# Optimization experiments

Measured on AMD Instinct MI355X. Metric: run time of the kernel, lower is better.

The kernel has to match this reference:

```python
import jax, jax.numpy as jnp
import numpy as np

B, L, T, H, NL, DFF, DIN = 4096, 64, 256, 8, 4, 1024, 6
HD = T // H
EPS = 1e-9


def setup_inputs() -> dict:
    key = jax.random.key(0)
    ks = jax.random.split(key, 12)
    s = 0.02
    inp = {
        "link_states": jax.random.uniform(ks[0], (B, L, DIN), jnp.float32) * 10.0,
        "link_W1": jax.random.normal(ks[1], (L, DIN, T), jnp.float32) * s,
        "link_b1": jnp.zeros((L, T), jnp.float32),
        "link_W2": jax.random.normal(ks[2], (L, T, T), jnp.float32) * s,
        "link_b2": jnp.zeros((L, T), jnp.float32),
        "Wqkv": jax.random.normal(ks[3], (NL, 3 * T, T), jnp.float32) * s,
        "bqkv": jnp.zeros((NL, 3 * T), jnp.float32),
        "Wo": jax.random.normal(ks[4], (NL, T, T), jnp.float32) * s,
        "bo": jnp.zeros((NL, T), jnp.float32),
        "ln1_g": jnp.ones((NL, T), jnp.float32),
        "ln1_b": jnp.zeros((NL, T), jnp.float32),
        "Wff1": jax.random.normal(ks[5], (NL, DFF, T), jnp.float32) * s,
        "bff1": jnp.zeros((NL, DFF), jnp.float32),
        "Wff2": jax.random.normal(ks[6], (NL, T, DFF), jnp.float32) * s,
        "bff2": jnp.zeros((NL, T), jnp.float32),
        "ln2_g": jnp.ones((NL, T), jnp.float32),
        "ln2_b": jnp.zeros((NL, T), jnp.float32),
        "head_W1": jax.random.normal(ks[7], (T, T), jnp.float32) * s,
        "head_b1": jnp.zeros((T,), jnp.float32),
        "head_W2": jax.random.normal(ks[8], (T, 1), jnp.float32) * s,
        "head_b2": jnp.zeros((1,), jnp.float32),
    }
    return inp


def _layernorm(x, g, b):
    m = x.mean(-1, keepdims=True)
    v = ((x - m) ** 2).mean(-1, keepdims=True)
    return (x - m) * jax.lax.rsqrt(v + 1e-5) * g + b


def _normalize_inputs(x):
    # x: [B, L, 6]
    prop = jnp.clip(x[:, :, 0], 0.0)
    tx = jnp.clip(x[:, :, 1], 0.0)
    sum_pt = prop + tx
    # torch.median returns lower-middle element for even L
    t_ref = jnp.sort(sum_pt, axis=1)[:, (L - 1) // 2][:, None]
    t_ref = jnp.clip(t_ref, 1e-6)
    f0 = prop / t_ref
    f1 = tx / t_ref
    f2 = x[:, :, 2]
    f3 = jnp.log1p(jnp.clip(x[:, :, 3], 0.0))
    f4 = jnp.log1p(jnp.clip(x[:, :, 4], 0.0) / t_ref)
    f5 = jnp.log1p(jnp.clip(x[:, :, 5], 0.0))
    head5 = jnp.stack([f0, f1, f2, f3, f4], axis=-1)  # [B,L,5]
    mean_a = head5.mean(axis=1, keepdims=True)
    std_a = head5.std(axis=1, keepdims=True) + EPS
    head5 = jnp.clip(head5, mean_a - 3.0 * std_a, mean_a + 3.0 * std_a)
    mean = head5.mean(axis=1, keepdims=True)
    std = head5.std(axis=1, keepdims=True) + EPS
    head5 = (head5 - mean) / std
    return jnp.concatenate([head5, f5[:, :, None]], axis=-1)


def _posenc():
    pos = jnp.arange(L, dtype=jnp.float32)[:, None]
    div = jnp.exp(-jnp.log(10000.0) * jnp.arange(0, T, 2, dtype=jnp.float32) / T)
    pe = jnp.zeros((L, T), jnp.float32)
    pe = pe.at[:, 0::2].set(jnp.sin(pos * div))
    pe = pe.at[:, 1::2].set(jnp.cos(pos * div))
    return pe


def _forward(link_states, link_W1, link_b1, link_W2, link_b2, Wqkv, bqkv, Wo, bo,
             ln1_g, ln1_b, Wff1, bff1, Wff2, bff2, ln2_g, ln2_b,
             head_W1, head_b1, head_W2, head_b2):
    x = _normalize_inputs(link_states)  # [B,L,6]
    # per-link (unshared) MLP encoders, batched as grouped matmuls
    h = jax.nn.relu(jnp.einsum('bld,ldt->blt', x, link_W1) + link_b1)
    tok = jnp.einsum('blt,lts->bls', h, link_W2) + link_b2  # [B,L,T]
    y = tok + _posenc()
    scale = 1.0 / np.sqrt(HD)
    for l in range(NL):
        qkv = y @ Wqkv[l].T + bqkv[l]  # [B,L,3T]
        q, k, v = jnp.split(qkv, 3, axis=-1)
        q = q.reshape(B, L, H, HD).transpose(0, 2, 1, 3)
        k = k.reshape(B, L, H, HD).transpose(0, 2, 1, 3)
        v = v.reshape(B, L, H, HD).transpose(0, 2, 1, 3)
        attn = jax.nn.softmax(jnp.einsum('bhqd,bhkd->bhqk', q, k) * scale, axis=-1)
        o = jnp.einsum('bhqk,bhkd->bhqd', attn, v).transpose(0, 2, 1, 3).reshape(B, L, T)
        o = o @ Wo[l].T + bo[l]
        y = _layernorm(y + o, ln1_g[l], ln1_b[l])
        ff = jax.nn.relu(y @ Wff1[l].T + bff1[l]) @ Wff2[l].T + bff2[l]
        y = _layernorm(y + ff, ln2_g[l], ln2_b[l])
    pooled = y.mean(axis=1)  # [B,T]
    hh = jax.nn.relu(pooled @ head_W1 + head_b1)
    values = (hh @ head_W2 + head_b2)[:, 0]  # [B]
    return values


def reference(link_states, link_W1, link_b1, link_W2, link_b2, Wqkv, bqkv, Wo, bo,
              ln1_g, ln1_b, Wff1, bff1, Wff2, bff2, ln2_g, ln2_b,
              head_W1, head_b1, head_W2, head_b2):
    return _forward(link_states, link_W1, link_b1, link_W2, link_b2, Wqkv, bqkv, Wo, bo,
                    ln1_g, ln1_b, Wff1, bff1, Wff2, bff2, ln2_g, ln2_b,
                    head_W1, head_b1, head_W2, head_b2)
```

## Files before the change

### kernel.cpp

```cpp
#include <hip/hip_runtime.h>
#include <cstddef>

#define B_   4096
#define L_   64
#define T_   256
#define H_   8
#define HD_  32
#define NL_  4
#define DFF_ 1024
#define DIN_ 6

typedef unsigned short ushort_t;
typedef __attribute__((ext_vector_type(8))) short bf16x8;
typedef __attribute__((ext_vector_type(4))) float f32x4;

__device__ __forceinline__ float wred_sum(float v) {
#pragma unroll
  for (int off = 32; off >= 1; off >>= 1) v += __shfl_xor(v, off, 64);
  return v;
}
__device__ __forceinline__ ushort_t f2bf(float f) {
  unsigned u = __builtin_bit_cast(unsigned, f);
  u += 0x7fffu + ((u >> 16) & 1u);
  return (ushort_t)(u >> 16);
}
__device__ __forceinline__ float bf2f(ushort_t h) {
  unsigned u = ((unsigned)h) << 16;
  return __builtin_bit_cast(float, u);
}
__device__ __forceinline__ unsigned pk2bf(float a, float b) {
  unsigned r;
  asm volatile("v_cvt_pk_bf16_f32 %0, %1, %2" : "=v"(r) : "v"(a), "v"(b));
  return r;
}
__device__ __forceinline__ void gl16(const ushort_t* g, const ushort_t* l) {
  __builtin_amdgcn_global_load_lds(
      (const __attribute__((address_space(1))) unsigned int*)g,
      (__attribute__((address_space(3))) unsigned int*)l, 16, 0, 0);
}

__global__ __launch_bounds__(256) void normalize_k(const float* __restrict__ xs,
                                                   float* __restrict__ xn) {
  const int w = threadIdx.x >> 6;
  const int b = blockIdx.x * 4 + w;
  const int l = threadIdx.x & 63;
  const float* x = xs + ((size_t)b * L_ + l) * DIN_;
  const float x0 = x[0], x1 = x[1], x2 = x[2], x3 = x[3], x4 = x[4], x5 = x[5];
  const float prop = fmaxf(x0, 0.f), tx = fmaxf(x1, 0.f);
  const float sp = prop + tx;

  __shared__ float sh[4][64];
  __shared__ float med_sh[4];
  sh[w][l] = sp;
  __syncthreads();
  int rk = 0;
#pragma unroll 8
  for (int j = 0; j < 64; ++j) {
    const float vj = sh[w][j];
    rk += (vj < sp) || (vj == sp && j < l);
  }
  if (rk == 31) med_sh[w] = sp;
  __syncthreads();
  const float t_ref = fmaxf(med_sh[w], 1e-6f);

  float f[5];
  f[0] = prop / t_ref;
  f[1] = tx / t_ref;
  f[2] = x2;
  f[3] = log1pf(fmaxf(x3, 0.f));
  f[4] = log1pf(fmaxf(x4, 0.f) / t_ref);
  const float f5 = log1pf(fmaxf(x5, 0.f));

  float* dst = xn + ((size_t)b * L_ + l) * DIN_;
#pragma unroll
  for (int i = 0; i < 5; ++i) {
    float v = f[i];
    float m = wred_sum(v) * (1.f / 64.f);
    float d = v - m;
    float sd = sqrtf(wred_sum(d * d) * (1.f / 64.f)) + 1e-9f;
    const float lo = m - 3.f * sd, hi = m + 3.f * sd;
    const float cv = fminf(fmaxf(v, lo), hi);
    const float m2 = wred_sum(cv) * (1.f / 64.f);
    const float d2 = cv - m2;
    const float sd2 = sqrtf(wred_sum(d2 * d2) * (1.f / 64.f)) + 1e-9f;
    dst[i] = (cv - m2) / sd2;
  }
  dst[5] = f5;
}

__global__ __launch_bounds__(256) void prep_k(
    const float* __restrict__ Wqkv, ushort_t* __restrict__ Wqkv16,
    const float* __restrict__ Wo,   ushort_t* __restrict__ Wo16,
    const float* __restrict__ Wff1, ushort_t* __restrict__ Wff116,
    const float* __restrict__ Wff2, ushort_t* __restrict__ Wff216,
    const float* __restrict__ W2,   ushort_t* __restrict__ W2T16,
    float* __restrict__ pe) {
  long idx = (long)blockIdx.x * 256 + threadIdx.x;
  if (idx < 786432) {
    const int NK = 196608;
    const int z = (int)(idx / NK), r = (int)(idx % NK);
    const int e = r & 7, li = (r >> 3) & 15, t = r >> 7;
    const int ks = t & 31, cb = t >> 5;
    Wqkv16[(size_t)z * NK + r] =
        f2bf(Wqkv[(size_t)z * NK + (size_t)(cb * 16 + li) * 256 + ks * 8 + e]);
    return;
  }
  idx -= 786432;
  if (idx < 262144) {
    const int NK = 65536;
    const int z = (int)(idx / NK), r = (int)(idx % NK);
    const int e = r & 7, li = (r >> 3) & 15, t = r >> 7;
    const int ks = t & 31, cb = t >> 5;
    Wo16[(size_t)z * NK + r] =
        f2bf(Wo[(size_t)z * NK + (size_t)(cb * 16 + li) * 256 + ks * 8 + e]);
    return;
  }
  idx -= 262144;
  if (idx < 1048576) {
    const int NK = 262144;
    const int z = (int)(idx / NK), r = (int)(idx % NK);
    const int e = r & 7, li = (r >> 3) & 15, t = r >> 7;
    const int ks = t & 31, cb = t >> 5;
    Wff116[(size_t)z * NK + r] =
        f2bf(Wff1[(size_t)z * NK + (size_t)(cb * 16 + li) * 256 + ks * 8 + e]);
    return;
  }
  idx -= 1048576;
  if (idx < 1048576) {
    const int NK = 262144;
    const int z = (int)(idx / NK), r = (int)(idx % NK);
    const int e = r & 7, li = (r >> 3) & 15, t = r >> 7;
    const int ks = t & 127, cb = t >> 7;
    Wff216[(size_t)z * NK + r] =
        f2bf(Wff2[(size_t)z * NK + (size_t)(cb * 16 + li) * 1024 + ks * 8 + e]);
    return;
  }
  idx -= 1048576;
  if (idx < 4194304) {
    const int l = (int)(idx >> 16), r = (int)(idx & 65535), s = r >> 8, t = r & 255;
    W2T16[idx] = f2bf(W2[((size_t)l << 16) | (t << 8) | s]);
    return;
  }
  idx -= 4194304;
  if (idx < 8192) {
    const int l = (int)(idx >> 7), i = (int)(idx & 127);
    const float div = expf(-9.210340371976184f * (2.0f * i) / 256.0f);
    const float ang = (float)l * div;
    pe[l * T_ + 2 * i]     = sinf(ang);
    pe[l * T_ + 2 * i + 1] = cosf(ang);
  }
}

__global__ __launch_bounds__(256) void link1_k(const float* __restrict__ xn,
                                               const float* __restrict__ W1,
                                               const float* __restrict__ b1,
                                               ushort_t* __restrict__ h,
                                               int Bc) {
  const size_t r0 = (size_t)blockIdx.x * 16;
  const int col = threadIdx.x;
#pragma unroll
  for (int i = 0; i < 16; ++i) {
    const size_t r = r0 + i;
    const int l = (int)(r & (L_ - 1));
    const size_t bloc = r >> 6;
    const float* x = xn + r * DIN_;
    float a = b1[l * T_ + col];
#pragma unroll
    for (int d = 0; d < DIN_; ++d)
      a = fmaf(x[d], W1[((size_t)l * DIN_ + d) * T_ + col], a);
    h[((size_t)l * Bc + bloc) * T_ + col] = f2bf(fmaxf(a, 0.f));
  }
}

__global__ __launch_bounds__(512) void linkgemm_k(
    const ushort_t* __restrict__ A,
    const ushort_t* __restrict__ W,
    const float* __restrict__ bias,
    const float* __restrict__ pe,
    float* __restrict__ y32, int Bc) {
  __shared__ ushort_t lA[2][4096];
  __shared__ ushort_t lB[2][8192];
  const int tid = threadIdx.x;
  const int lane = tid & 63, w = tid >> 6;
  const int wr = w >> 2, wc = w & 3;
  const size_t b0 = (size_t)blockIdx.x * 128;
  const int l = blockIdx.z;
  const ushort_t* Az = A + ((size_t)l * Bc + b0) * 256;
  const ushort_t* Wz = W + (size_t)l * 65536;

  const int sm = tid >> 6, sks = (tid >> 4) & 3, srr = tid & 15;

  auto stage = [&](int buf, int kt) {
    gl16(Az + (size_t)(16 * sm + srr) * 256 + kt + sks * 8,
         &lA[buf][(tid & ~63) * 8]);
#pragma unroll
    for (int rd = 0; rd < 2; ++rd) {
      const int nb = sm + rd * 8;
      gl16(Wz + (size_t)(nb * 16 + srr) * 256 + kt + sks * 8,
           &lB[buf][rd * 4096 + (tid & ~63) * 8]);
    }
  };

  f32x4 acc[4][4];
#pragma unroll
  for (int mi = 0; mi < 4; ++mi)
#pragma unroll
    for (int ni = 0; ni < 4; ++ni) acc[mi][ni] = (f32x4){0.f, 0.f, 0.f, 0.f};

  stage(0, 0);
  asm volatile("s_waitcnt vmcnt(0)" ::: "memory");
  __syncthreads();
  int cur = 0;
  for (int t = 0; t < 8; ++t) {
    if (t + 1 < 8) stage(cur ^ 1, (t + 1) << 5);
    bf16x8 af[4], bfr[4];
#pragma unroll
    for (int mi = 0; mi < 4; ++mi)
      af[mi] = *(const bf16x8*)&lA[cur][((wr * 4 + mi) * 64 + lane) * 8];
#pragma unroll
    for (int ni = 0; ni < 4; ++ni)
      bfr[ni] = *(const bf16x8*)&lB[cur][((wc * 4 + ni) * 64 + lane) * 8];
#pragma unroll
    for (int mi = 0; mi < 4; ++mi)
#pragma unroll
      for (int ni = 0; ni < 4; ++ni)
        acc[mi][ni] = __builtin_amdgcn_mfma_f32_16x16x32_bf16(
            af[mi], bfr[ni], acc[mi][ni], 0, 0, 0);
    asm volatile("s_waitcnt vmcnt(0)" ::: "memory");
    __syncthreads();
    cur ^= 1;
  }

  const int r_in = (lane >> 4) * 4;
  const int c_in = lane & 15;
#pragma unroll
  for (int ni = 0; ni < 4; ++ni) {
    const int cg = wc * 64 + ni * 16 + c_in;
    const float bs = bias[l * 256 + cg] + pe[l * 256 + cg];
#pragma unroll
    for (int mi = 0; mi < 4; ++mi) {
#pragma unroll
      for (int rg = 0; rg < 4; ++rg) {
        const size_t bg = b0 + wr * 64 + mi * 16 + r_in + rg;
        y32[bg * 16384 + l * 256 + cg] = acc[mi][ni][rg] + bs;
      }
    }
  }
}

template <int LAST>
__global__ __launch_bounds__(256, 2) void layer_k(
    float* __restrict__ y32,
    const ushort_t* __restrict__ Wq, const float* __restrict__ bqkv,
    const ushort_t* __restrict__ Wo, const float* __restrict__ bo,
    const float* __restrict__ ln1g, const float* __restrict__ ln1b,
    const ushort_t* __restrict__ Wf1, const float* __restrict__ bf1,
    const ushort_t* __restrict__ Wf2, const float* __restrict__ bf2,
    const float* __restrict__ ln2g, const float* __restrict__ ln2b,
    float* __restrict__ pool) {
  __shared__ ushort_t yF[16384];
  __shared__ ushort_t sc[18432];
  __shared__ float red[4][2][64];
  const int b = blockIdx.x;
  const int tid = threadIdx.x, lane = tid & 63, w = tid >> 6;
  const int li = lane & 15, g = lane >> 4;
  const size_t row0 = (size_t)b * 64;
  const float scale = 0.17677669529663687f;
  ushort_t* bufw = sc + w * 2304;
  ushort_t* vtw  = sc + 9216 + w * 2304;
  ushort_t* zF   = sc;

#pragma unroll
  for (int j = 0; j < 8; ++j) {
    const int u = j * 256 + tid;
    const int row = u & 63, ks = u >> 6;
    const float* src = y32 + (row0 + row) * 256 + ks * 8;
    const float4 a = *(const float4*)src;
    const float4 c = *(const float4*)(src + 4);
    uint4 v;
    v.x = pk2bf(a.x, a.y);
    v.y = pk2bf(a.z, a.w);
    v.z = pk2bf(c.x, c.y);
    v.w = pk2bf(c.z, c.w);
    *(uint4*)&yF[(((row >> 4) * 32 + ks) * 16 + (row & 15)) * 8] = v;
  }
  __syncthreads();

  f32x4 oa2[2][4][2];
#pragma unroll
  for (int hi = 0; hi < 2; ++hi) {
    const int h = w * 2 + hi, hoff = h * 32;

    f32x4 acc[3][2][4];
#pragma unroll
    for (int m = 0; m < 3; ++m)
#pragma unroll
      for (int n = 0; n < 2; ++n)
#pragma unroll
        for (int mi = 0; mi < 4; ++mi) acc[m][n][mi] = (f32x4){0.f, 0.f, 0.f, 0.f};
    __builtin_amdgcn_s_setprio(1);
#pragma unroll
    for (int kt = 0; kt < 8; ++kt) {
      bf16x8 af[4];
#pragma unroll
      for (int mi = 0; mi < 4; ++mi)
        af[mi] = *(const bf16x8*)&yF[((mi * 32 + kt * 4 + g) * 16 + li) * 8];
      bf16x8 bw[3][2];
#pragma unroll
      for (int m = 0; m < 3; ++m)
#pragma unroll
        for (int n = 0; n < 2; ++n)
          bw[m][n] = *(const bf16x8*)(Wq +
              (size_t)(((m * 16 + 2 * h + n) * 32 + kt * 4 + g) * 16 + li) * 8);
#pragma unroll
      for (int m = 0; m < 3; ++m)
#pragma unroll
        for (int n = 0; n < 2; ++n)
#pragma unroll
          for (int mi = 0; mi < 4; ++mi)
            acc[m][n][mi] = __builtin_amdgcn_mfma_f32_16x16x32_bf16(
                af[mi], bw[m][n], acc[m][n][mi], 0, 0, 0);
    }
    __builtin_amdgcn_s_setprio(0);
    float bs[3][2];
#pragma unroll
    for (int m = 0; m < 3; ++m)
#pragma unroll
      for (int n = 0; n < 2; ++n) bs[m][n] = bqkv[m * 256 + hoff + 16 * n + li];

#pragma unroll
    for (int n = 0; n < 2; ++n)
#pragma unroll
      for (int mi = 0; mi < 4; ++mi) {
        const unsigned p0 = pk2bf(acc[0][n][mi][0] + bs[0][n],
                                  acc[0][n][mi][1] + bs[0][n]);
        const unsigned p1 = pk2bf(acc[0][n][mi][2] + bs[0][n],
                                  acc[0][n][mi][3] + bs[0][n]);
        const int base = (16 * mi + 4 * g) * 36 + 16 * n + li;
        bufw[base]       = (ushort_t)p0;
        bufw[base + 36]  = (ushort_t)(p0 >> 16);
        bufw[base + 72]  = (ushort_t)p1;
        bufw[base + 108] = (ushort_t)(p1 >> 16);
      }
    bf16x8 qb[4];
#pragma unroll
    for (int ni = 0; ni < 4; ++ni)
      qb[ni] = *(const bf16x8*)&bufw[(16 * ni + li) * 36 + g * 8];

#pragma unroll
    for (int n = 0; n < 2; ++n)
#pragma unroll
      for (int mi = 0; mi < 4; ++mi) {
        const unsigned p0 = pk2bf(acc[1][n][mi][0] + bs[1][n],
                                  acc[1][n][mi][1] + bs[1][n]);
        const unsigned p1 = pk2bf(acc[1][n][mi][2] + bs[1][n],
                                  acc[1][n][mi][3] + bs[1][n]);
        const int base = (16 * mi + 4 * g) * 36 + 16 * n + li;
        bufw[base]       = (ushort_t)p0;
        bufw[base + 36]  = (ushort_t)(p0 >> 16);
        bufw[base + 72]  = (ushort_t)p1;
        bufw[base + 108] = (ushort_t)(p1 >> 16);
      }
    bf16x8 ka[4];
#pragma unroll
    for (int mi = 0; mi < 4; ++mi)
      ka[mi] = *(const bf16x8*)&bufw[(16 * mi + li) * 36 + g * 8];

#pragma unroll
    for (int n = 0; n < 2; ++n)
#pragma unroll
      for (int mi = 0; mi < 4; ++mi) {
        const unsigned p0 = pk2bf(acc[2][n][mi][0] + bs[2][n],
                                  acc[2][n][mi][1] + bs[2][n]);
        const unsigned p1 = pk2bf(acc[2][n][mi][2] + bs[2][n],
                                  acc[2][n][mi][3] + bs[2][n]);
        *(uint2*)&vtw[(16 * n + li) * 72 + 16 * mi + 4 * g] = make_uint2(p0, p1);
      }
    bf16x8 vb[2][2];
#pragma unroll
    for (int ks = 0; ks < 2; ++ks)
#pragma unroll
      for (int n2 = 0; n2 < 2; ++n2)
        vb[ks][n2] = *(const bf16x8*)&vtw[(16 * n2 + li) * 72 + ks * 32 + g * 8];

#pragma unroll
    for (int mi = 0; mi < 4; ++mi)
#pragma unroll
      for (int n2 = 0; n2 < 2; ++n2) oa2[hi][mi][n2] = (f32x4){0.f, 0.f, 0.f, 0.f};

#pragma unroll
    for (int half = 0; half < 2; ++half) {
      f32x4 s[4][2];
      __builtin_amdgcn_s_setprio(1);
#pragma unroll
      for (int mi = 0; mi < 4; ++mi)
#pragma unroll
        for (int nn = 0; nn < 2; ++nn)
          s[mi][nn] = __builtin_amdgcn_mfma_f32_16x16x32_bf16(
              ka[mi], qb[2 * half + nn], (f32x4){0.f, 0.f, 0.f, 0.f}, 0, 0, 0);
      __builtin_amdgcn_s_setprio(0);

#pragma unroll
      for (int nn = 0; nn < 2; ++nn) {
        float mx = -3.4e38f;
#pragma unroll
        for (int mi = 0; mi < 4; ++mi)
#pragma unroll
          for (int r = 0; r < 4; ++r) {
            s[mi][nn][r] *= scale;
            mx = fmaxf(mx, s[mi][nn][r]);
          }
        mx = fmaxf(mx, __shfl_xor(mx, 16, 64));
        mx = fmaxf(mx, __shfl_xor(mx, 32, 64));
        float sum = 0.f;
#pragma unroll
        for (int mi = 0; mi < 4; ++mi)
#pragma unroll
          for (int r = 0; r < 4; ++r) {
            const float e = expf(s[mi][nn][r] - mx);
            s[mi][nn][r] = e;
            sum += e;
          }
        sum += __shfl_xor(sum, 16, 64);
        sum += __shfl_xor(sum, 32, 64);
        const float inv = 1.f / sum;
        const int qrow = 16 * nn + li;
#pragma unroll
        for (int mi = 0; mi < 4; ++mi) {
          const unsigned lo = pk2bf(s[mi][nn][0] * inv, s[mi][nn][1] * inv);
          const unsigned hi2 = pk2bf(s[mi][nn][2] * inv, s[mi][nn][3] * inv);
          *(uint2*)&bufw[qrow * 72 + 16 * mi + 4 * g] = make_uint2(lo, hi2);
        }
      }

      __builtin_amdgcn_s_setprio(1);
#pragma unroll
      for (int ks = 0; ks < 2; ++ks) {
        bf16x8 pa[2];
#pragma unroll
        for (int m2 = 0; m2 < 2; ++m2)
          pa[m2] = *(const bf16x8*)&bufw[(16 * m2 + li) * 72 + ks * 32 + g * 8];
#pragma unroll
        for (int m2 = 0; m2 < 2; ++m2)
#pragma unroll
          for (int n2 = 0; n2 < 2; ++n2)
            oa2[hi][2 * half + m2][n2] = __builtin_amdgcn_mfma_f32_16x16x32_bf16(
                pa[m2], vb[ks][n2], oa2[hi][2 * half + m2][n2], 0, 0, 0);
      }
      __builtin_amdgcn_s_setprio(0);
    }
  }

  __syncthreads();
#pragma unroll
  for (int hi = 0; hi < 2; ++hi) {
    const int hoff = (2 * w + hi) * 32;
#pragma unroll
    for (int mi = 0; mi < 4; ++mi)
#pragma unroll
      for (int n2 = 0; n2 < 2; ++n2) {
        const unsigned p0 = pk2bf(oa2[hi][mi][n2][0], oa2[hi][mi][n2][1]);
        const unsigned p1 = pk2bf(oa2[hi][mi][n2][2], oa2[hi][mi][n2][3]);
        const int col = hoff + 16 * n2 + li;
        const int base = ((mi * 32 + (col >> 3)) * 16 + 4 * g) * 8 + (col & 7);
        yF[base]      = (ushort_t)p0;
        yF[base + 8]  = (ushort_t)(p0 >> 16);
        yF[base + 16] = (ushort_t)p1;
        yF[base + 24] = (ushort_t)(p1 >> 16);
      }
  }
  __syncthreads();

  f32x4 acc[4][4];
#pragma unroll
  for (int mi = 0; mi < 4; ++mi)
#pragma unroll
    for (int ni = 0; ni < 4; ++ni) acc[mi][ni] = (f32x4){0.f, 0.f, 0.f, 0.f};
  __builtin_amdgcn_s_setprio(1);
#pragma unroll
  for (int kt = 0; kt < 8; ++kt) {
    bf16x8 af[4], bfr[4];
#pragma unroll
    for (int mi = 0; mi < 4; ++mi)
      af[mi] = *(const bf16x8*)&yF[((mi * 32 + kt * 4 + g) * 16 + li) * 8];
#pragma unroll
    for (int ni = 0; ni < 4; ++ni)
      bfr[ni] = *(const bf16x8*)(Wo +
          (size_t)(((4 * w + ni) * 32 + kt * 4 + g) * 16 + li) * 8);
#pragma unroll
    for (int mi = 0; mi < 4; ++mi)
#pragma unroll
      for (int ni = 0; ni < 4; ++ni)
        acc[mi][ni] = __builtin_amdgcn_mfma_f32_16x16x32_bf16(
            af[mi], bfr[ni], acc[mi][ni], 0, 0, 0);
  }
  __builtin_amdgcn_s_setprio(0);

  const int r_in = (lane >> 4) * 4;
  const int c_in = lane & 15;
  float y1r[4][4][4];
#pragma unroll
  for (int mi = 0; mi < 4; ++mi) {
#pragma unroll
    for (int rg = 0; rg < 4; ++rg) {
      const int row_l = 16 * mi + r_in + rg;
      float s1 = 0.f, s2 = 0.f;
#pragma unroll
      for (int ni = 0; ni < 4; ++ni) {
        const int cg = 64 * w + 16 * ni + c_in;
        const float zv = acc[mi][ni][rg] + bo[cg] + y32[(row0 + row_l) * 256 + cg];
        acc[mi][ni][rg] = zv;
        s1 += zv;
        s2 += zv * zv;
      }
#pragma unroll
      for (int off = 1; off <= 8; off <<= 1) {
        s1 += __shfl_xor(s1, off, 64);
        s2 += __shfl_xor(s2, off, 64);
      }
      if (c_in == 0) {
        red[w][0][row_l] = s1;
        red[w][1][row_l] = s2;
      }
    }
  }
  __syncthreads();
#pragma unroll
  for (int mi = 0; mi < 4; ++mi) {
#pragma unroll
    for (int rg = 0; rg < 4; ++rg) {
      const int row_l = 16 * mi + r_in + rg;
      const float S1 = red[0][0][row_l] + red[1][0][row_l] + red[2][0][row_l] + red[3][0][row_l];
      const float S2 = red[0][1][row_l] + red[1][1][row_l] + red[2][1][row_l] + red[3][1][row_l];
      const float m = S1 * (1.f / 256.f);
      const float var = S2 * (1.f / 256.f) - m * m;
      const float rs = rsqrtf(var + 1e-5f);
      float tv[4];
#pragma unroll
      for (int ni = 0; ni < 4; ++ni) {
        const int cg = 64 * w + 16 * ni + c_in;
        tv[ni] = (acc[mi][ni][rg] - m) * rs * ln1g[cg] + ln1b[cg];
        y1r[mi][ni][rg] = tv[ni];
      }
      const unsigned p0 = pk2bf(tv[0], tv[1]);
      const unsigned p1 = pk2bf(tv[2], tv[3]);
#pragma unroll
      for (int ni = 0; ni < 4; ++ni) {
        const int cg = 64 * w + 16 * ni + c_in;
        const unsigned pk = (ni < 2) ? p0 : p1;
        const ushort_t hv = (ni & 1) ? (ushort_t)(pk >> 16) : (ushort_t)pk;
        yF[((mi * 32 + (cg >> 3)) * 16 + (row_l & 15)) * 8 + (cg & 7)] = hv;
      }
    }
  }
  __syncthreads();

  f32x4 acc2[4][4];
#pragma unroll
  for (int mi = 0; mi < 4; ++mi)
#pragma unroll
    for (int ni = 0; ni < 4; ++ni) acc2[mi][ni] = (f32x4){0.f, 0.f, 0.f, 0.f};

#pragma unroll 1
  for (int q = 0; q < 4; ++q) {
#pragma unroll 1
    for (int p = 0; p < 2; ++p) {
      f32x4 acc1[4][2];
#pragma unroll
      for (int mi = 0; mi < 4; ++mi)
#pragma unroll
        for (int n = 0; n < 2; ++n) acc1[mi][n] = (f32x4){0.f, 0.f, 0.f, 0.f};
      __builtin_amdgcn_s_setprio(1);
#pragma unroll
      for (int kt = 0; kt < 8; ++kt) {
        bf16x8 af[4], bw[2];
#pragma unroll
        for (int mi = 0; mi < 4; ++mi)
          af[mi] = *(const bf16x8*)&yF[((mi * 32 + kt * 4 + g) * 16 + li) * 8];
#pragma unroll
        for (int n = 0; n < 2; ++n)
          bw[n] = *(const bf16x8*)(Wf1 +
              (size_t)(((16 * q + 4 * w + 2 * p + n) * 32 + kt * 4 + g) * 16 + li) * 8);
#pragma unroll
        for (int mi = 0; mi < 4; ++mi)
#pragma unroll
          for (int n = 0; n < 2; ++n)
            acc1[mi][n] = __builtin_amdgcn_mfma_f32_16x16x32_bf16(
                af[mi], bw[n], acc1[mi][n], 0, 0, 0);
      }
      __builtin_amdgcn_s_setprio(0);
      if (q && p == 0) __syncthreads();
#pragma unroll
      for (int n = 0; n < 2; ++n) {
        const int kk = 64 * w + 32 * p + 16 * n + li;
        const float bb = bf1[256 * q + kk];
#pragma unroll
        for (int mi = 0; mi < 4; ++mi) {
          const unsigned p0 = pk2bf(fmaxf(acc1[mi][n][0] + bb, 0.f),
                                    fmaxf(acc1[mi][n][1] + bb, 0.f));
          const unsigned p1 = pk2bf(fmaxf(acc1[mi][n][2] + bb, 0.f),
                                    fmaxf(acc1[mi][n][3] + bb, 0.f));
          const int base = ((mi * 32 + (kk >> 3)) * 16 + 4 * g) * 8 + (kk & 7);
          zF[base]      = (ushort_t)p0;
          zF[base + 8]  = (ushort_t)(p0 >> 16);
          zF[base + 16] = (ushort_t)p1;
          zF[base + 24] = (ushort_t)(p1 >> 16);
        }
      }
    }
    __syncthreads();
    __builtin_amdgcn_s_setprio(1);
#pragma unroll
    for (int kt = 0; kt < 8; ++kt) {
      bf16x8 af2[4], bw2[4];
#pragma unroll
      for (int mi = 0; mi < 4; ++mi)
        af2[mi] = *(const bf16x8*)&zF[((mi * 32 + kt * 4 + g) * 16 + li) * 8];
#pragma unroll
      for (int ni = 0; ni < 4; ++ni)
        bw2[ni] = *(const bf16x8*)(Wf2 +
            (size_t)(((4 * w + ni) * 128 + 32 * q + kt * 4 + g) * 16 + li) * 8);
#pragma unroll
      for (int mi = 0; mi < 4; ++mi)
#pragma unroll
        for (int ni = 0; ni < 4; ++ni)
          acc2[mi][ni] = __builtin_amdgcn_mfma_f32_16x16x32_bf16(
              af2[mi], bw2[ni], acc2[mi][ni], 0, 0, 0);
    }
    __builtin_amdgcn_s_setprio(0);
  }

#pragma unroll
  for (int mi = 0; mi < 4; ++mi) {
#pragma unroll
    for (int rg = 0; rg < 4; ++rg) {
      const int row_l = 16 * mi + r_in + rg;
      float s1 = 0.f, s2 = 0.f;
#pragma unroll
      for (int ni = 0; ni < 4; ++ni) {
        const int cg = 64 * w + 16 * ni + c_in;
        const float zv = acc2[mi][ni][rg] + bf2[cg] + y1r[mi][ni][rg];
        acc2[mi][ni][rg] = zv;
        s1 += zv;
        s2 += zv * zv;
      }
#pragma unroll
      for (int off = 1; off <= 8; off <<= 1) {
        s1 += __shfl_xor(s1, off, 64);
        s2 += __shfl_xor(s2, off, 64);
      }
      if (c_in == 0) {
        red[w][0][row_l] = s1;
        red[w][1][row_l] = s2;
      }
    }
  }
  __syncthreads();
  float colsum[4] = {0.f, 0.f, 0.f, 0.f};
#pragma unroll
  for (int mi = 0; mi < 4; ++mi) {
#pragma unroll
    for (int rg = 0; rg < 4; ++rg) {
      const int row_l = 16 * mi + r_in + rg;
      const float S1 = red[0][0][row_l] + red[1][0][row_l] + red[2][0][row_l] + red[3][0][row_l];
      const float S2 = red[0][1][row_l] + red[1][1][row_l] + red[2][1][row_l] + red[3][1][row_l];
      const float m = S1 * (1.f / 256.f);
      const float var = S2 * (1.f / 256.f) - m * m;
      const float rs = rsqrtf(var + 1e-5f);
#pragma unroll
      for (int ni = 0; ni < 4; ++ni) {
        const int cg = 64 * w + 16 * ni + c_in;
        const float v = (acc2[mi][ni][rg] - m) * rs * ln2g[cg] + ln2b[cg];
        if constexpr (LAST) {
          colsum[ni] += v;
        } else {
          y32[(row0 + row_l) * 256 + cg] = v;
        }
      }
    }
  }
  if constexpr (LAST) {
#pragma unroll
    for (int ni = 0; ni < 4; ++ni) {
      float s = colsum[ni];
      s += __shfl_xor(s, 16, 64);
      s += __shfl_xor(s, 32, 64);
      if (g == 0) pool[(size_t)b * 256 + 64 * w + 16 * ni + c_in] = s * (1.f / 64.f);
    }
  }
}

__global__ __launch_bounds__(256) void headgemm_k(
    const float* __restrict__ A, const float* __restrict__ Wt,
    const float* __restrict__ bias, float* __restrict__ out) {
  const int tid = threadIdx.x;
  const int tx = tid & 63, ty = tid >> 6;
  const int cfull = tx * 4;
  const size_t b0 = (size_t)blockIdx.x * 64;

  __shared__ float At[256][68];

  float4 acc[16];
#pragma unroll
  for (int r = 0; r < 16; ++r) acc[r] = make_float4(0.f, 0.f, 0.f, 0.f);
  const int r0 = ty * 16;

  {
    const int rr = tid >> 6;
    const int k4 = (tid & 63) * 4;
#pragma unroll
    for (int p = 0; p < 16; ++p) {
      const int r = p * 4 + rr;
      const float4 v = *(const float4*)(A + (b0 + r) * 256 + k4);
      At[k4 + 0][r] = v.x;
      At[k4 + 1][r] = v.y;
      At[k4 + 2][r] = v.z;
      At[k4 + 3][r] = v.w;
    }
  }
  __syncthreads();
  const float* wp = Wt + cfull;
#pragma unroll 2
  for (int k = 0; k < 256; ++k) {
    const float4 w = *(const float4*)wp;
    wp += 256;
    const float4* ar = (const float4*)(&At[k][r0]);
    const float4 a0 = ar[0], a1 = ar[1], a2 = ar[2], a3 = ar[3];
    const float av[16] = {a0.x, a0.y, a0.z, a0.w, a1.x, a1.y, a1.z, a1.w,
                          a2.x, a2.y, a2.z, a2.w, a3.x, a3.y, a3.z, a3.w};
#pragma unroll
    for (int r = 0; r < 16; ++r) {
      acc[r].x = fmaf(av[r], w.x, acc[r].x);
      acc[r].y = fmaf(av[r], w.y, acc[r].y);
      acc[r].z = fmaf(av[r], w.z, acc[r].z);
      acc[r].w = fmaf(av[r], w.w, acc[r].w);
    }
  }
  const float4 bb = *(const float4*)(bias + cfull);
#pragma unroll
  for (int r = 0; r < 16; ++r) {
    const size_t row = b0 + r0 + r;
    float4 o;
    o.x = fmaxf(acc[r].x + bb.x, 0.f);
    o.y = fmaxf(acc[r].y + bb.y, 0.f);
    o.z = fmaxf(acc[r].z + bb.z, 0.f);
    o.w = fmaxf(acc[r].w + bb.w, 0.f);
    *(float4*)(out + row * 256 + cfull) = o;
  }
}

__global__ __launch_bounds__(64) void head2_k(const float* __restrict__ hh,
                                              const float* __restrict__ W2,
                                              const float* __restrict__ b2,
                                              float* __restrict__ out) {
  const size_t b = blockIdx.x;
  const int lane = threadIdx.x;
  const float4 hv = *(const float4*)(hh + b * T_ + lane * 4);
  const float4 wv = *(const float4*)(W2 + lane * 4);
  float s = hv.x * wv.x + hv.y * wv.y + hv.z * wv.z + hv.w * wv.w;
  s = wred_sum(s);
  if (lane == 0) out[b] = s + b2[0];
}

extern "C" void kernel_launch(void* const* d_in, const int* in_sizes, int n_in,
                              void* d_out, int out_size, void* d_ws, size_t ws_size,
                              hipStream_t stream) {
  const float* link_states = (const float*)d_in[0];
  const float* link_W1 = (const float*)d_in[1];
  const float* link_b1 = (const float*)d_in[2];
  const float* link_W2 = (const float*)d_in[3];
  const float* link_b2 = (const float*)d_in[4];
  const float* Wqkv = (const float*)d_in[5];
  const float* bqkv = (const float*)d_in[6];
  const float* Wo = (const float*)d_in[7];
  const float* bo = (const float*)d_in[8];
  const float* ln1_g = (const float*)d_in[9];
  const float* ln1_b = (const float*)d_in[10];
  const float* Wff1 = (const float*)d_in[11];
  const float* bff1 = (const float*)d_in[12];
  const float* Wff2 = (const float*)d_in[13];
  const float* bff2 = (const float*)d_in[14];
  const float* ln2_g = (const float*)d_in[15];
  const float* ln2_b = (const float*)d_in[16];
  const float* head_W1 = (const float*)d_in[17];
  const float* head_b1 = (const float*)d_in[18];
  const float* head_W2 = (const float*)d_in[19];
  const float* head_b2 = (const float*)d_in[20];

  char* base = (char*)d_ws;
  size_t off = 0;
  auto alloc = [&](size_t bytes) -> char* {
    char* p = base + off;
    off = (off + bytes + 255) & ~(size_t)255;
    return p;
  };

  ushort_t* Wqkv16 = (ushort_t*)alloc((size_t)NL_ * 768 * 256 * 2);
  ushort_t* Wo16   = (ushort_t*)alloc((size_t)NL_ * 256 * 256 * 2);
  ushort_t* Wff116 = (ushort_t*)alloc((size_t)NL_ * 1024 * 256 * 2);
  ushort_t* Wff216 = (ushort_t*)alloc((size_t)NL_ * 256 * 1024 * 2);
  ushort_t* W2T16  = (ushort_t*)alloc((size_t)L_ * 256 * 256 * 2);
  float* pe     = (float*)alloc((size_t)L_ * T_ * 4);
  float* xn     = (float*)alloc((size_t)B_ * L_ * DIN_ * 4);
  float* pooled = (float*)alloc((size_t)B_ * T_ * 4);
  float* hh     = (float*)alloc((size_t)B_ * T_ * 4);

  const size_t fixed_end = off;
  const size_t availB = (ws_size > fixed_end + 65536) ? (ws_size - fixed_end - 65536) : 0;
  int NC = 1;
  while (NC < 32 && (size_t)(B_ / NC) * 98304ull > availB) NC <<= 1;
  const int Bc = B_ / NC;

  float*    y32  = (float*)alloc((size_t)Bc * L_ * T_ * 4);
  ushort_t* hbuf = (ushort_t*)alloc((size_t)Bc * L_ * T_ * 2);

  prep_k<<<28704, 256, 0, stream>>>(Wqkv, Wqkv16, Wo, Wo16, Wff1, Wff116,
                                    Wff2, Wff216, link_W2, W2T16, pe);
  normalize_k<<<B_ / 4, 256, 0, stream>>>(link_states, xn);

  for (int c = 0; c < NC; ++c) {
    const size_t bs = (size_t)c * Bc;

    link1_k<<<(Bc * L_) / 16, 256, 0, stream>>>(xn + bs * L_ * DIN_, link_W1,
                                                link_b1, hbuf, Bc);
    linkgemm_k<<<dim3(Bc / 128, 1, L_), 512, 0, stream>>>(
        hbuf, W2T16, link_b2, pe, y32, Bc);

    for (int l = 0; l < NL_ - 1; ++l) {
      layer_k<0><<<dim3(Bc, 1, 1), 256, 0, stream>>>(
          y32,
          Wqkv16 + (size_t)l * 768 * 256, bqkv + l * 768,
          Wo16 + (size_t)l * 256 * 256, bo + l * 256,
          ln1_g + l * 256, ln1_b + l * 256,
          Wff116 + (size_t)l * 1024 * 256, bff1 + l * 1024,
          Wff216 + (size_t)l * 256 * 1024, bff2 + l * 256,
          ln2_g + l * 256, ln2_b + l * 256, nullptr);
    }
    {
      const int l = NL_ - 1;
      layer_k<1><<<dim3(Bc, 1, 1), 256, 0, stream>>>(
          y32,
          Wqkv16 + (size_t)l * 768 * 256, bqkv + l * 768,
          Wo16 + (size_t)l * 256 * 256, bo + l * 256,
          ln1_g + l * 256, ln1_b + l * 256,
          Wff116 + (size_t)l * 1024 * 256, bff1 + l * 1024,
          Wff216 + (size_t)l * 256 * 1024, bff2 + l * 256,
          ln2_g + l * 256, ln2_b + l * 256, pooled + bs * T_);
    }
  }

  headgemm_k<<<B_ / 64, 256, 0, stream>>>(pooled, head_W1, head_b1, hh);
  head2_k<<<B_, 64, 0, stream>>>(hh, head_W2, head_b2, (float*)d_out);
}
```

Before: 3.527 ms.

## Fuse pairs of transformer layers into one kernel keeping activations on-chip

Merges two consecutive encoder layers into a single kernel launch. Between the two layers the residual stream stays in registers (yres) and in the bf16 LDS tile, so the fp32 activation round trip through global memory between layers is avoided, and the launch count halves. The cost is higher register pressure from holding the residual in registers across the whole layer, which under the 2-blocks-per-CU launch bound may cause spills.

Measured after the change: 6.624 ms. +87.8%, slower.

```diff
diff --git a/kernel.cpp b/kernel.cpp
--- a/kernel.cpp
+++ b/kernel.cpp
@@ -249,14 +249,14 @@
 }
 
 template <int LAST>
-__global__ __launch_bounds__(256, 2) void layer_k(
+__global__ __launch_bounds__(256, 2) void layers2_k(
     float* __restrict__ y32,
-    const ushort_t* __restrict__ Wq, const float* __restrict__ bqkv,
-    const ushort_t* __restrict__ Wo, const float* __restrict__ bo,
-    const float* __restrict__ ln1g, const float* __restrict__ ln1b,
-    const ushort_t* __restrict__ Wf1, const float* __restrict__ bf1,
-    const ushort_t* __restrict__ Wf2, const float* __restrict__ bf2,
-    const float* __restrict__ ln2g, const float* __restrict__ ln2b,
+    const ushort_t* __restrict__ Wq0, const float* __restrict__ bqkv0,
+    const ushort_t* __restrict__ Wo0, const float* __restrict__ bo0,
+    const float* __restrict__ ln1g0, const float* __restrict__ ln1b0,
+    const ushort_t* __restrict__ Wf10, const float* __restrict__ bf10,
+    const ushort_t* __restrict__ Wf20, const float* __restrict__ bf20,
+    const float* __restrict__ ln2g0, const float* __restrict__ ln2b0,
     float* __restrict__ pool) {
   __shared__ ushort_t yF[16384];
   __shared__ ushort_t sc[18432];
@@ -270,6 +270,9 @@
   ushort_t* vtw  = sc + 9216 + w * 2304;
   ushort_t* zF   = sc;
 
+  const int r_in = (lane >> 4) * 4;
+  const int c_in = lane & 15;
+
 #pragma unroll
   for (int j = 0; j < 8; ++j) {
     const int u = j * 256 + tid;
@@ -284,408 +287,465 @@
     v.w = pk2bf(c.z, c.w);
     *(uint4*)&yF[(((row >> 4) * 32 + ks) * 16 + (row & 15)) * 8] = v;
   }
+  float yres[4][4][4];
+#pragma unroll
+  for (int mi = 0; mi < 4; ++mi)
+#pragma unroll
+    for (int rg = 0; rg < 4; ++rg) {
+      const int row_l = 16 * mi + r_in + rg;
+#pragma unroll
+      for (int ni = 0; ni < 4; ++ni) {
+        const int cg = 64 * w + 16 * ni + c_in;
+        yres[mi][ni][rg] = y32[(row0 + row_l) * 256 + cg];
+      }
+    }
   __syncthreads();
 
-  f32x4 oa2[2][4][2];
-#pragma unroll
-  for (int hi = 0; hi < 2; ++hi) {
-    const int h = w * 2 + hi, hoff = h * 32;
-
-    f32x4 acc[3][2][4];
-#pragma unroll
-    for (int m = 0; m < 3; ++m)
+#pragma unroll 1
+  for (int l2 = 0; l2 < 2; ++l2) {
+    const ushort_t* Wq   = Wq0  + (size_t)l2 * 768 * 256;
+    const float*    bqkv = bqkv0 + l2 * 768;
+    const ushort_t* Wo   = Wo0  + (size_t)l2 * 256 * 256;
+    const float*    bo   = bo0  + l2 * 256;
+    const float*    ln1g = ln1g0 + l2 * 256;
+    const float*    ln1b = ln1b0 + l2 * 256;
+    const ushort_t* Wf1  = Wf10 + (size_t)l2 * 1024 * 256;
+    const float*    bf1  = bf10 + l2 * 1024;
+    const ushort_t* Wf2  = Wf20 + (size_t)l2 * 256 * 1024;
+    const float*    bf2  = bf20 + l2 * 256;
+    const float*    ln2g = ln2g0 + l2 * 256;
+    const float*    ln2b = ln2b0 + l2 * 256;
+
+    f32x4 oa2[2][4][2];
+#pragma unroll
+    for (int hi = 0; hi < 2; ++hi) {
+      const int h = w * 2 + hi, hoff = h * 32;
+
+      f32x4 acc[3][2][4];
+#pragma unroll
+      for (int m = 0; m < 3; ++m)
+#pragma unroll
+        for (int n = 0; n < 2; ++n)
+#pragma unroll
+          for (int mi = 0; mi < 4; ++mi) acc[m][n][mi] = (f32x4){0.f, 0.f, 0.f, 0.f};
+      __builtin_amdgcn_s_setprio(1);
+#pragma unroll
+      for (int kt = 0; kt < 8; ++kt) {
+        bf16x8 af[4];
+#pragma unroll
+        for (int mi = 0; mi < 4; ++mi)
+          af[mi] = *(const bf16x8*)&yF[((mi * 32 + kt * 4 + g) * 16 + li) * 8];
+        bf16x8 bw[3][2];
+#pragma unroll
+        for (int m = 0; m < 3; ++m)
+#pragma unroll
+          for (int n = 0; n < 2; ++n)
+            bw[m][n] = *(const bf16x8*)(Wq +
+                (size_t)(((m * 16 + 2 * h + n) * 32 + kt * 4 + g) * 16 + li) * 8);
+#pragma unroll
+        for (int m = 0; m < 3; ++m)
+#pragma unroll
+          for (int n = 0; n < 2; ++n)
+#pragma unroll
+            for (int mi = 0; mi < 4; ++mi)
+              acc[m][n][mi] = __builtin_amdgcn_mfma_f32_16x16x32_bf16(
+                  af[mi], bw[m][n], acc[m][n][mi], 0, 0, 0);
+      }
+      __builtin_amdgcn_s_setprio(0);
+      float bs[3][2];
+#pragma unroll
+      for (int m = 0; m < 3; ++m)
+#pragma unroll
+        for (int n = 0; n < 2; ++n) bs[m][n] = bqkv[m * 256 + hoff + 16 * n + li];
+
 #pragma unroll
       for (int n = 0; n < 2; ++n)
 #pragma unroll
-        for (int mi = 0; mi < 4; ++mi) acc[m][n][mi] = (f32x4){0.f, 0.f, 0.f, 0.f};
+        for (int mi = 0; mi < 4; ++mi) {
+          const unsigned p0 = pk2bf(acc[0][n][mi][0] + bs[0][n],
+                                    acc[0][n][mi][1] + bs[0][n]);
+          const unsigned p1 = pk2bf(acc[0][n][mi][2] + bs[0][n],
+                                    acc[0][n][mi][3] + bs[0][n]);
+          const int base = (16 * mi + 4 * g) * 36 + 16 * n + li;
+          bufw[base]       = (ushort_t)p0;
+          bufw[base + 36]  = (ushort_t)(p0 >> 16);
+          bufw[base + 72]  = (ushort_t)p1;
+          bufw[base + 108] = (ushort_t)(p1 >> 16);
+        }
+      bf16x8 qb[4];
+#pragma unroll
+      for (int ni = 0; ni < 4; ++ni)
+        qb[ni] = *(const bf16x8*)&bufw[(16 * ni + li) * 36 + g * 8];
+
+#pragma unroll
+      for (int n = 0; n < 2; ++n)
+#pragma unroll
+        for (int mi = 0; mi < 4; ++mi) {
+          const unsigned p0 = pk2bf(acc[1][n][mi][0] + bs[1][n],
+                                    acc[1][n][mi][1] + bs[1][n]);
+          const unsigned p1 = pk2bf(acc[1][n][mi][2] + bs[1][n],
+                                    acc[1][n][mi][3] + bs[1][n]);
+          const int base = (16 * mi + 4 * g) * 36 + 16 * n + li;
+          bufw[base]       = (ushort_t)p0;
+          bufw[base + 36]  = (ushort_t)(p0 >> 16);
+          bufw[base + 72]  = (ushort_t)p1;
+          bufw[base + 108] = (ushort_t)(p1 >> 16);
+        }
+      bf16x8 ka[4];
+#pragma unroll
+      for (int mi = 0; mi < 4; ++mi)
+        ka[mi] = *(const bf16x8*)&bufw[(16 * mi + li) * 36 + g * 8];
+
+#pragma unroll
+      for (int n = 0; n < 2; ++n)
+#pragma unroll
+        for (int mi = 0; mi < 4; ++mi) {
+          const unsigned p0 = pk2bf(acc[2][n][mi][0] + bs[2][n],
+                                    acc[2][n][mi][1] + bs[2][n]);
+          const unsigned p1 = pk2bf(acc[2][n][mi][2] + bs[2][n],
+                                    acc[2][n][mi][3] + bs[2][n]);
+          *(uint2*)&vtw[(16 * n + li) * 72 + 16 * mi + 4 * g] = make_uint2(p0, p1);
+        }
+      bf16x8 vb[2][2];
+#pragma unroll
+      for (int ks = 0; ks < 2; ++ks)
+#pragma unroll
+        for (int n2 = 0; n2 < 2; ++n2)
+          vb[ks][n2] = *(const bf16x8*)&vtw[(16 * n2 + li) * 72 + ks * 32 + g * 8];
+
+#pragma unroll
+      for (int mi = 0; mi < 4; ++mi)
+#pragma unroll
+        for (int n2 = 0; n2 < 2; ++n2) oa2[hi][mi][n2] = (f32x4){0.f, 0.f, 0.f, 0.f};
+
+#pragma unroll
+      for (int half = 0; half < 2; ++half) {
+        f32x4 s[4][2];
+        __builtin_amdgcn_s_setprio(1);
+#pragma unroll
+        for (int mi = 0; mi < 4; ++mi)
+#pragma unroll
+          for (int nn = 0; nn < 2; ++nn)
+            s[mi][nn] = __builtin_amdgcn_mfma_f32_16x16x32_bf16(
+                ka[mi], qb[2 * half + nn], (f32x4){0.f, 0.f, 0.f, 0.f}, 0, 0, 0);
+        __builtin_amdgcn_s_setprio(0);
+
+#pragma unroll
+        for (int nn = 0; nn < 2; ++nn) {
+          float mx = -3.4e38f;
+#pragma unroll
+          for (int mi = 0; mi < 4; ++mi)
+#pragma unroll
+            for (int r = 0; r < 4; ++r) {
+              s[mi][nn][r] *= scale;
+              mx = fmaxf(mx, s[mi][nn][r]);
+            }
+          mx = fmaxf(mx, __shfl_xor(mx, 16, 64));
+          mx = fmaxf(mx, __shfl_xor(mx, 32, 64));
+          float sum = 0.f;
+#pragma unroll
+          for (int mi = 0; mi < 4; ++mi)
+#pragma unroll
+            for (int r = 0; r < 4; ++r) {
+              const float e = expf(s[mi][nn][r] - mx);
+              s[mi][nn][r] = e;
+              sum += e;
+            }
+          sum += __shfl_xor(sum, 16, 64);
+          sum += __shfl_xor(sum, 32, 64);
+          const float inv = 1.f / sum;
+          const int qrow = 16 * nn + li;
+#pragma unroll
+          for (int mi = 0; mi < 4; ++mi) {
+            const unsigned lo = pk2bf(s[mi][nn][0] * inv, s[mi][nn][1] * inv);
+            const unsigned hi2 = pk2bf(s[mi][nn][2] * inv, s[mi][nn][3] * inv);
+            *(uint2*)&bufw[qrow * 72 + 16 * mi + 4 * g] = make_uint2(lo, hi2);
+          }
+        }
+
+        __builtin_amdgcn_s_setprio(1);
+#pragma unroll
+        for (int ks = 0; ks < 2; ++ks) {
+          bf16x8 pa[2];
+#pragma unroll
+          for (int m2 = 0; m2 < 2; ++m2)
+            pa[m2] = *(const bf16x8*)&bufw[(16 * m2 + li) * 72 + ks * 32 + g * 8];
+#pragma unroll
+          for (int m2 = 0; m2 < 2; ++m2)
+#pragma unroll
+            for (int n2 = 0; n2 < 2; ++n2)
+              oa2[hi][2 * half + m2][n2] = __builtin_amdgcn_mfma_f32_16x16x32_bf16(
+                  pa[m2], vb[ks][n2], oa2[hi][2 * half + m2][n2], 0, 0, 0);
+        }
+        __builtin_amdgcn_s_setprio(0);
+      }
+    }
+
+    __syncthreads();
+#pragma unroll
+    for (int hi = 0; hi < 2; ++hi) {
+      const int hoff = (2 * w + hi) * 32;
+#pragma unroll
+      for (int mi = 0; mi < 4; ++mi)
+#pragma unroll
+        for (int n2 = 0; n2 < 2; ++n2) {
+          const unsigned p0 = pk2bf(oa2[hi][mi][n2][0], oa2[hi][mi][n2][1]);
+          const unsigned p1 = pk2bf(oa2[hi][mi][n2][2], oa2[hi][mi][n2][3]);
+          const int col = hoff + 16 * n2 + li;
+          const int base = ((mi * 32 + (col >> 3)) * 16 + 4 * g) * 8 + (col & 7);
+          yF[base]      = (ushort_t)p0;
+          yF[base + 8]  = (ushort_t)(p0 >> 16);
+          yF[base + 16] = (ushort_t)p1;
+          yF[base + 24] = (ushort_t)(p1 >> 16);
+        }
+    }
+    __syncthreads();
+
+    f32x4 acc[4][4];
+#pragma unroll
+    for (int mi = 0; mi < 4; ++mi)
+#pragma unroll
+      for (int ni = 0; ni < 4; ++ni) acc[mi][ni] = (f32x4){0.f, 0.f, 0.f, 0.f};
     __builtin_amdgcn_s_setprio(1);
 #pragma unroll
     for (int kt = 0; kt < 8; ++kt) {
-      bf16x8 af[4];
+      bf16x8 af[4], bfr[4];
 #pragma unroll
       for (int mi = 0; mi < 4; ++mi)
         af[mi] = *(const bf16x8*)&yF[((mi * 32 + kt * 4 + g) * 16 + li) * 8];
-      bf16x8 bw[3][2];
-#pragma unroll
-      for (int m = 0; m < 3; ++m)
-#pragma unroll
-        for (int n = 0; n < 2; ++n)
-          bw[m][n] = *(const bf16x8*)(Wq +
-              (size_t)(((m * 16 + 2 * h + n) * 32 + kt * 4 + g) * 16 + li) * 8);
-#pragma unroll
-      for (int m = 0; m < 3; ++m)
-#pragma unroll
-        for (int n = 0; n < 2; ++n)
+#pragma unroll
+      for (int ni = 0; ni < 4; ++ni)
+        bfr[ni] = *(const bf16x8*)(Wo +
+            (size_t)(((4 * w + ni) * 32 + kt * 4 + g) * 16 + li) * 8);
+#pragma unroll
+      for (int mi = 0; mi < 4; ++mi)
+#pragma unroll
+        for (int ni = 0; ni < 4; ++ni)
+          acc[mi][ni] = __builtin_amdgcn_mfma_f32_16x16x32_bf16(
+              af[mi], bfr[ni], acc[mi][ni], 0, 0, 0);
+    }
+    __builtin_amdgcn_s_setprio(0);
+
+#pragma unroll
+    for (int mi = 0; mi < 4; ++mi) {
+#pragma unroll
+      for (int rg = 0; rg < 4; ++rg) {
+        const int row_l = 16 * mi + r_in + rg;
+        float s1 = 0.f, s2 = 0.f;
+#pragma unroll
+        for (int ni = 0; ni < 4; ++ni) {
+          const int cg = 64 * w + 16 * ni + c_in;
+          const float zv = acc[mi][ni][rg] + bo[cg] + yres[mi][ni][rg];
+          acc[mi][ni][rg] = zv;
+          s1 += zv;
+          s2 += zv * zv;
+        }
+#pragma unroll
+        for (int off = 1; off <= 8; off <<= 1) {
+          s1 += __shfl_xor(s1, off, 64);
+          s2 += __shfl_xor(s2, off, 64);
+        }
+        if (c_in == 0) {
+          red[w][0][row_l] = s1;
+          red[w][1][row_l] = s2;
+        }
+      }
+    }
+    __syncthreads();
+#pragma unroll
+    for (int mi = 0; mi < 4; ++mi) {
+#pragma unroll
+      for (int rg = 0; rg < 4; ++rg) {
+        const int row_l = 16 * mi + r_in + rg;
+        const float S1 = red[0][0][row_l] + red[1][0][row_l] + red[2][0][row_l] + red[3][0][row_l];
+        const float S2 = red[0][1][row_l] + red[1][1][row_l] + red[2][1][row_l] + red[3][1][row_l];
+        const float m = S1 * (1.f / 256.f);
+        const float var = S2 * (1.f / 256.f) - m * m;
+        const float rs = rsqrtf(var + 1e-5f);
+        float tv[4];
+#pragma unroll
+        for (int ni = 0; ni < 4; ++ni) {
+          const int cg = 64 * w + 16 * ni + c_in;
+          tv[ni] = (acc[mi][ni][rg] - m) * rs * ln1g[cg] + ln1b[cg];
+          yres[mi][ni][rg] = tv[ni];
+        }
+        const unsigned p0 = pk2bf(tv[0], tv[1]);
+        const unsigned p1 = pk2bf(tv[2], tv[3]);
+#pragma unroll
+        for (int ni = 0; ni < 4; ++ni) {
+          const int cg = 64 * w + 16 * ni + c_in;
+          const unsigned pk = (ni < 2) ? p0 : p1;
+          const ushort_t hv = (ni & 1) ? (ushort_t)(pk >> 16) : (ushort_t)pk;
+          yF[((mi * 32 + (cg >> 3)) * 16 + (row_l & 15)) * 8 + (cg & 7)] = hv;
+        }
+      }
+    }
+    __syncthreads();
+
+    f32x4 acc2[4][4];
+#pragma unroll
+    for (int mi = 0; mi < 4; ++mi)
+#pragma unroll
+      for (int ni = 0; ni < 4; ++ni) acc2[mi][ni] = (f32x4){0.f, 0.f, 0.f, 0.f};
+
+#pragma unroll 1
+    for (int q = 0; q < 4; ++q) {
+#pragma unroll 1
+      for (int p = 0; p < 2; ++p) {
+        f32x4 acc1[4][2];
+#pragma unroll
+        for (int mi = 0; mi < 4; ++mi)
+#pragma unroll
+          for (int n = 0; n < 2; ++n) acc1[mi][n] = (f32x4){0.f, 0.f, 0.f, 0.f};
+        __builtin_amdgcn_s_setprio(1);
+#pragma unroll
+        for (int kt = 0; kt < 8; ++kt) {
+          bf16x8 af[4], bw[2];
 #pragma unroll
           for (int mi = 0; mi < 4; ++mi)
-            acc[m][n][mi] = __builtin_amdgcn_mfma_f32_16x16x32_bf16(
-                af[mi], bw[m][n], acc[m][n][mi], 0, 0, 0);
-    }
-    __builtin_amdgcn_s_setprio(0);
-    float bs[3][2];
-#pragma unroll
-    for (int m = 0; m < 3; ++m)
-#pragma unroll
-      for (int n = 0; n < 2; ++n) bs[m][n] = bqkv[m * 256 + hoff + 16 * n + li];
-
-#pragma unroll
-    for (int n = 0; n < 2; ++n)
+            af[mi] = *(const bf16x8*)&yF[((mi * 32 + kt * 4 + g) * 16 + li) * 8];
+#pragma unroll
+          for (int n = 0; n < 2; ++n)
+            bw[n] = *(const bf16x8*)(Wf1 +
+                (size_t)(((16 * q + 4 * w + 2 * p + n) * 32 + kt * 4 + g) * 16 + li) * 8);
+#pragma unroll
+          for (int mi = 0; mi < 4; ++mi)
+#pragma unroll
+            for (int n = 0; n < 2; ++n)
+              acc1[mi][n] = __builtin_amdgcn_mfma_f32_16x16x32_bf16(
+                  af[mi], bw[n], acc1[mi][n], 0, 0, 0);
+        }
+        __builtin_amdgcn_s_setprio(0);
+        if (q && p == 0) __syncthreads();
+#pragma unroll
+        for (int n = 0; n < 2; ++n) {
+          const int kk = 64 * w + 32 * p + 16 * n + li;
+          const float bb = bf1[256 * q + kk];
+#pragma unroll
+          for (int mi = 0; mi < 4; ++mi) {
+            const unsigned p0 = pk2bf(fmaxf(acc1[mi][n][0] + bb, 0.f),
+                                      fmaxf(acc1[mi][n][1] + bb, 0.f));
+            const unsigned p1 = pk2bf(fmaxf(acc1[mi][n][2] + bb, 0.f),
+                                      fmaxf(acc1[mi][n][3] + bb, 0.f));
+            const int base = ((mi * 32 + (kk >> 3)) * 16 + 4 * g) * 8 + (kk & 7);
+            zF[base]      = (ushort_t)p0;
+            zF[base + 8]  = (ushort_t)(p0 >> 16);
+            zF[base + 16] = (ushort_t)p1;
+            zF[base + 24] = (ushort_t)(p1 >> 16);
+          }
+        }
+      }
+      __syncthreads();
+      __builtin_amdgcn_s_setprio(1);
+#pragma unroll
+      for (int kt = 0; kt < 8; ++kt) {
+        bf16x8 af2[4], bw2[4];
+#pragma unroll
+        for (int mi = 0; mi < 4; ++mi)
+          af2[mi] = *(const bf16x8*)&zF[((mi * 32 + kt * 4 + g) * 16 + li) * 8];
+#pragma unroll
+        for (int ni = 0; ni < 4; ++ni)
+          bw2[ni] = *(const bf16x8*)(Wf2 +
+              (size_t)(((4 * w + ni) * 128 + 32 * q + kt * 4 + g) * 16 + li) * 8);
+#pragma unroll
+        for (int mi = 0; mi < 4; ++mi)
+#pragma unroll
+          for (int ni = 0; ni < 4; ++ni)
+            acc2[mi][ni] = __builtin_amdgcn_mfma_f32_16x16x32_bf16(
+                af2[mi], bw2[ni], acc2[mi][ni], 0, 0, 0);
+      }
+      __builtin_amdgcn_s_setprio(0);
+    }
+
+#pragma unroll
+    for (int mi = 0; mi < 4; ++mi) {
+#pragma unroll
+      for (int rg = 0; rg < 4; ++rg) {
+        const int row_l = 16 * mi + r_in + rg;
+        float s1 = 0.f, s2 = 0.f;
+#pragma unroll
+        for (int ni = 0; ni < 4; ++ni) {
+          const int cg = 64 * w + 16 * ni + c_in;
+          const float zv = acc2[mi][ni][rg] + bf2[cg] + yres[mi][ni][rg];
+          acc2[mi][ni][rg] = zv;
+          s1 += zv;
+          s2 += zv * zv;
+        }
+#pragma unroll
+        for (int off = 1; off <= 8; off <<= 1) {
+          s1 += __shfl_xor(s1, off, 64);
+          s2 += __shfl_xor(s2, off, 64);
+        }
+        if (c_in == 0) {
+          red[w][0][row_l] = s1;
+          red[w][1][row_l] = s2;
+        }
+      }
+    }
+    __syncthreads();
+    if (l2 == 1) {
+      float colsum[4] = {0.f, 0.f, 0.f, 0.f};
 #pragma unroll
       for (int mi = 0; mi < 4; ++mi) {
-        const unsigned p0 = pk2bf(acc[0][n][mi][0] + bs[0][n],
-                                  acc[0][n][mi][1] + bs[0][n]);
-        const unsigned p1 = pk2bf(acc[0][n][mi][2] + bs[0][n],
-                                  acc[0][n][mi][3] + bs[0][n]);
-        const int base = (16 * mi + 4 * g) * 36 + 16 * n + li;
-        bufw[base]       = (ushort_t)p0;
-        bufw[base + 36]  = (ushort_t)(p0 >> 16);
-        bufw[base + 72]  = (ushort_t)p1;
-        bufw[base + 108] = (ushort_t)(p1 >> 16);
-      }
-    bf16x8 qb[4];
-#pragma unroll
-    for (int ni = 0; ni < 4; ++ni)
-      qb[ni] = *(const bf16x8*)&bufw[(16 * ni + li) * 36 + g * 8];
-
-#pragma unroll
-    for (int n = 0; n < 2; ++n)
+#pragma unroll
+        for (int rg = 0; rg < 4; ++rg) {
+          const int row_l = 16 * mi + r_in + rg;
+          const float S1 = red[0][0][row_l] + red[1][0][row_l] + red[2][0][row_l] + red[3][0][row_l];
+          const float S2 = red[0][1][row_l] + red[1][1][row_l] + red[2][1][row_l] + red[3][1][row_l];
+          const float m = S1 * (1.f / 256.f);
+          const float var = S2 * (1.f / 256.f) - m * m;
+          const float rs = rsqrtf(var + 1e-5f);
+#pragma unroll
+          for (int ni = 0; ni < 4; ++ni) {
+            const int cg = 64 * w + 16 * ni + c_in;
+            const float v = (acc2[mi][ni][rg] - m) * rs * ln2g[cg] + ln2b[cg];
+            if constexpr (LAST) {
+              colsum[ni] += v;
+            } else {
+              y32[(row0 + row_l) * 256 + cg] = v;
+            }
+          }
+        }
+      }
+      if constexpr (LAST) {
+#pragma unroll
+        for (int ni = 0; ni < 4; ++ni) {
+          float s = colsum[ni];
+          s += __shfl_xor(s, 16, 64);
+          s += __shfl_xor(s, 32, 64);
+          if (g == 0) pool[(size_t)b * 256 + 64 * w + 16 * ni + c_in] = s * (1.f / 64.f);
+        }
+      }
+    } else {
 #pragma unroll
       for (int mi = 0; mi < 4; ++mi) {
-        const unsigned p0 = pk2bf(acc[1][n][mi][0] + bs[1][n],
-                                  acc[1][n][mi][1] + bs[1][n]);
-        const unsigned p1 = pk2bf(acc[1][n][mi][2] + bs[1][n],
-                                  acc[1][n][mi][3] + bs[1][n]);
-        const int base = (16 * mi + 4 * g) * 36 + 16 * n + li;
-        bufw[base]       = (ushort_t)p0;
-        bufw[base + 36]  = (ushort_t)(p0 >> 16);
-        bufw[base + 72]  = (ushort_t)p1;
-        bufw[base + 108] = (ushort_t)(p1 >> 16);
-      }
-    bf16x8 ka[4];
-#pragma unroll
-    for (int mi = 0; mi < 4; ++mi)
-      ka[mi] = *(const bf16x8*)&bufw[(16 * mi + li) * 36 + g * 8];
-
-#pragma unroll
-    for (int n = 0; n < 2; ++n)
-#pragma unroll
-      for (int mi = 0; mi < 4; ++mi) {
-        const unsigned p0 = pk2bf(acc[2][n][mi][0] + bs[2][n],
-                                  acc[2][n][mi][1] + bs[2][n]);
-        const unsigned p1 = pk2bf(acc[2][n][mi][2] + bs[2][n],
-                                  acc[2][n][mi][3] + bs[2][n]);
-        *(uint2*)&vtw[(16 * n + li) * 72 + 16 * mi + 4 * g] = make_uint2(p0, p1);
-      }
-    bf16x8 vb[2][2];
-#pragma unroll
-    for (int ks = 0; ks < 2; ++ks)
-#pragma unroll
-      for (int n2 = 0; n2 < 2; ++n2)
-        vb[ks][n2] = *(const bf16x8*)&vtw[(16 * n2 + li) * 72 + ks * 32 + g * 8];
-
-#pragma unroll
-    for (int mi = 0; mi < 4; ++mi)
-#pragma unroll
-      for (int n2 = 0; n2 < 2; ++n2) oa2[hi][mi][n2] = (f32x4){0.f, 0.f, 0.f, 0.f};
-
-#pragma unroll
-    for (int half = 0; half < 2; ++half) {
-      f32x4 s[4][2];
-      __builtin_amdgcn_s_setprio(1);
-#pragma unroll
-      for (int mi = 0; mi < 4; ++mi)
-#pragma unroll
-        for (int nn = 0; nn < 2; ++nn)
-          s[mi][nn] = __builtin_amdgcn_mfma_f32_16x16x32_bf16(
-              ka[mi], qb[2 * half + nn], (f32x4){0.f, 0.f, 0.f, 0.f}, 0, 0, 0);
-      __builtin_amdgcn_s_setprio(0);
-
-#pragma unroll
-      for (int nn = 0; nn < 2; ++nn) {
-        float mx = -3.4e38f;
-#pragma unroll
-        for (int mi = 0; mi < 4; ++mi)
-#pragma unroll
-          for (int r = 0; r < 4; ++r) {
-            s[mi][nn][r] *= scale;
-            mx = fmaxf(mx, s[mi][nn][r]);
+#pragma unroll
+        for (int rg = 0; rg < 4; ++rg) {
+          const int row_l = 16 * mi + r_in + rg;
+          const float S1 = red[0][0][row_l] + red[1][0][row_l] + red[2][0][row_l] + red[3][0][row_l];
+          const float S2 = red[0][1][row_l] + red[1][1][row_l] + red[2][1][row_l] + red[3][1][row_l];
+          const float m = S1 * (1.f / 256.f);
+          const float var = S2 * (1.f / 256.f) - m * m;
+          const float rs = rsqrtf(var + 1e-5f);
+          float tv[4];
+#pragma unroll
+          for (int ni = 0; ni < 4; ++ni) {
+            const int cg = 64 * w + 16 * ni + c_in;
+            tv[ni] = (acc2[mi][ni][rg] - m) * rs * ln2g[cg] + ln2b[cg];
+            yres[mi][ni][rg] = tv[ni];
           }
-        mx = fmaxf(mx, __shfl_xor(mx, 16, 64));
-        mx = fmaxf(mx, __shfl_xor(mx, 32, 64));
-        float sum = 0.f;
-#pragma unroll
-        for (int mi = 0; mi < 4; ++mi)
-#pragma unroll
-          for (int r = 0; r < 4; ++r) {
-            const float e = expf(s[mi][nn][r] - mx);
-            s[mi][nn][r] = e;
-            sum += e;
+          const unsigned p0 = pk2bf(tv[0], tv[1]);
+          const unsigned p1 = pk2bf(tv[2], tv[3]);
+#pragma unroll
+          for (int ni = 0; ni < 4; ++ni) {
+            const int cg = 64 * w + 16 * ni + c_in;
+            const unsigned pk = (ni < 2) ? p0 : p1;
+            const ushort_t hv = (ni & 1) ? (ushort_t)(pk >> 16) : (ushort_t)pk;
+            yF[((mi * 32 + (cg >> 3)) * 16 + (row_l & 15)) * 8 + (cg & 7)] = hv;
           }
-        sum += __shfl_xor(sum, 16, 64);
-        sum += __shfl_xor(sum, 32, 64);
-        const float inv = 1.f / sum;
-        const int qrow = 16 * nn + li;
-#pragma unroll
-        for (int mi = 0; mi < 4; ++mi) {
-          const unsigned lo = pk2bf(s[mi][nn][0] * inv, s[mi][nn][1] * inv);
-          const unsigned hi2 = pk2bf(s[mi][nn][2] * inv, s[mi][nn][3] * inv);
-          *(uint2*)&bufw[qrow * 72 + 16 * mi + 4 * g] = make_uint2(lo, hi2);
-        }
-      }
-
-      __builtin_amdgcn_s_setprio(1);
-#pragma unroll
-      for (int ks = 0; ks < 2; ++ks) {
-        bf16x8 pa[2];
-#pragma unroll
-        for (int m2 = 0; m2 < 2; ++m2)
-          pa[m2] = *(const bf16x8*)&bufw[(16 * m2 + li) * 72 + ks * 32 + g * 8];
-#pragma unroll
-        for (int m2 = 0; m2 < 2; ++m2)
-#pragma unroll
-          for (int n2 = 0; n2 < 2; ++n2)
-            oa2[hi][2 * half + m2][n2] = __builtin_amdgcn_mfma_f32_16x16x32_bf16(
-                pa[m2], vb[ks][n2], oa2[hi][2 * half + m2][n2], 0, 0, 0);
-      }
-      __builtin_amdgcn_s_setprio(0);
-    }
-  }
-
-  __syncthreads();
-#pragma unroll
-  for (int hi = 0; hi < 2; ++hi) {
-    const int hoff = (2 * w + hi) * 32;
-#pragma unroll
-    for (int mi = 0; mi < 4; ++mi)
-#pragma unroll
-      for (int n2 = 0; n2 < 2; ++n2) {
-        const unsigned p0 = pk2bf(oa2[hi][mi][n2][0], oa2[hi][mi][n2][1]);
-        const unsigned p1 = pk2bf(oa2[hi][mi][n2][2], oa2[hi][mi][n2][3]);
-        const int col = hoff + 16 * n2 + li;
-        const int base = ((mi * 32 + (col >> 3)) * 16 + 4 * g) * 8 + (col & 7);
-        yF[base]      = (ushort_t)p0;
-        yF[base + 8]  = (ushort_t)(p0 >> 16);
-        yF[base + 16] = (ushort_t)p1;
-        yF[base + 24] = (ushort_t)(p1 >> 16);
-      }
-  }
-  __syncthreads();
-
-  f32x4 acc[4][4];
-#pragma unroll
-  for (int mi = 0; mi < 4; ++mi)
-#pragma unroll
-    for (int ni = 0; ni < 4; ++ni) acc[mi][ni] = (f32x4){0.f, 0.f, 0.f, 0.f};
-  __builtin_amdgcn_s_setprio(1);
-#pragma unroll
-  for (int kt = 0; kt < 8; ++kt) {
-    bf16x8 af[4], bfr[4];
-#pragma unroll
-    for (int mi = 0; mi < 4; ++mi)
-      af[mi] = *(const bf16x8*)&yF[((mi * 32 + kt * 4 + g) * 16 + li) * 8];
-#pragma unroll
-    for (int ni = 0; ni < 4; ++ni)
-      bfr[ni] = *(const bf16x8*)(Wo +
-          (size_t)(((4 * w + ni) * 32 + kt * 4 + g) * 16 + li) * 8);
-#pragma unroll
-    for (int mi = 0; mi < 4; ++mi)
-#pragma unroll
-      for (int ni = 0; ni < 4; ++ni)
-        acc[mi][ni] = __builtin_amdgcn_mfma_f32_16x16x32_bf16(
-            af[mi], bfr[ni], acc[mi][ni], 0, 0, 0);
-  }
-  __builtin_amdgcn_s_setprio(0);
-
-  const int r_in = (lane >> 4) * 4;
-  const int c_in = lane & 15;
-  float y1r[4][4][4];
-#pragma unroll
-  for (int mi = 0; mi < 4; ++mi) {
-#pragma unroll
-    for (int rg = 0; rg < 4; ++rg) {
-      const int row_l = 16 * mi + r_in + rg;
-      float s1 = 0.f, s2 = 0.f;
-#pragma unroll
-      for (int ni = 0; ni < 4; ++ni) {
-        const int cg = 64 * w + 16 * ni + c_in;
-        const float zv = acc[mi][ni][rg] + bo[cg] + y32[(row0 + row_l) * 256 + cg];
-        acc[mi][ni][rg] = zv;
-        s1 += zv;
-        s2 += zv * zv;
-      }
-#pragma unroll
-      for (int off = 1; off <= 8; off <<= 1) {
-        s1 += __shfl_xor(s1, off, 64);
-        s2 += __shfl_xor(s2, off, 64);
-      }
-      if (c_in == 0) {
-        red[w][0][row_l] = s1;
-        red[w][1][row_l] = s2;
-      }
-    }
-  }
-  __syncthreads();
-#pragma unroll
-  for (int mi = 0; mi < 4; ++mi) {
-#pragma unroll
-    for (int rg = 0; rg < 4; ++rg) {
-      const int row_l = 16 * mi + r_in + rg;
-      const float S1 = red[0][0][row_l] + red[1][0][row_l] + red[2][0][row_l] + red[3][0][row_l];
-      const float S2 = red[0][1][row_l] + red[1][1][row_l] + red[2][1][row_l] + red[3][1][row_l];
-      const float m = S1 * (1.f / 256.f);
-      const float var = S2 * (1.f / 256.f) - m * m;
-      const float rs = rsqrtf(var + 1e-5f);
-      float tv[4];
-#pragma unroll
-      for (int ni = 0; ni < 4; ++ni) {
-        const int cg = 64 * w + 16 * ni + c_in;
-        tv[ni] = (acc[mi][ni][rg] - m) * rs * ln1g[cg] + ln1b[cg];
-        y1r[mi][ni][rg] = tv[ni];
-      }
-      const unsigned p0 = pk2bf(tv[0], tv[1]);
-      const unsigned p1 = pk2bf(tv[2], tv[3]);
-#pragma unroll
-      for (int ni = 0; ni < 4; ++ni) {
-        const int cg = 64 * w + 16 * ni + c_in;
-        const unsigned pk = (ni < 2) ? p0 : p1;
-        const ushort_t hv = (ni & 1) ? (ushort_t)(pk >> 16) : (ushort_t)pk;
-        yF[((mi * 32 + (cg >> 3)) * 16 + (row_l & 15)) * 8 + (cg & 7)] = hv;
-      }
-    }
-  }
-  __syncthreads();
-
-  f32x4 acc2[4][4];
-#pragma unroll
-  for (int mi = 0; mi < 4; ++mi)
-#pragma unroll
-    for (int ni = 0; ni < 4; ++ni) acc2[mi][ni] = (f32x4){0.f, 0.f, 0.f, 0.f};
-
-#pragma unroll 1
-  for (int q = 0; q < 4; ++q) {
-#pragma unroll 1
-    for (int p = 0; p < 2; ++p) {
-      f32x4 acc1[4][2];
-#pragma unroll
-      for (int mi = 0; mi < 4; ++mi)
-#pragma unroll
-        for (int n = 0; n < 2; ++n) acc1[mi][n] = (f32x4){0.f, 0.f, 0.f, 0.f};
-      __builtin_amdgcn_s_setprio(1);
-#pragma unroll
-      for (int kt = 0; kt < 8; ++kt) {
-        bf16x8 af[4], bw[2];
-#pragma unroll
-        for (int mi = 0; mi < 4; ++mi)
-          af[mi] = *(const bf16x8*)&yF[((mi * 32 + kt * 4 + g) * 16 + li) * 8];
-#pragma unroll
-        for (int n = 0; n < 2; ++n)
-          bw[n] = *(const bf16x8*)(Wf1 +
-              (size_t)(((16 * q + 4 * w + 2 * p + n) * 32 + kt * 4 + g) * 16 + li) * 8);
-#pragma unroll
-        for (int mi = 0; mi < 4; ++mi)
-#pragma unroll
-          for (int n = 0; n < 2; ++n)
-            acc1[mi][n] = __builtin_amdgcn_mfma_f32_16x16x32_bf16(
-                af[mi], bw[n], acc1[mi][n], 0, 0, 0);
-      }
-      __builtin_amdgcn_s_setprio(0);
-      if (q && p == 0) __syncthreads();
-#pragma unroll
-      for (int n = 0; n < 2; ++n) {
-        const int kk = 64 * w + 32 * p + 16 * n + li;
-        const float bb = bf1[256 * q + kk];
-#pragma unroll
-        for (int mi = 0; mi < 4; ++mi) {
-          const unsigned p0 = pk2bf(fmaxf(acc1[mi][n][0] + bb, 0.f),
-                                    fmaxf(acc1[mi][n][1] + bb, 0.f));
-          const unsigned p1 = pk2bf(fmaxf(acc1[mi][n][2] + bb, 0.f),
-                                    fmaxf(acc1[mi][n][3] + bb, 0.f));
-          const int base = ((mi * 32 + (kk >> 3)) * 16 + 4 * g) * 8 + (kk & 7);
-          zF[base]      = (ushort_t)p0;
-          zF[base + 8]  = (ushort_t)(p0 >> 16);
-          zF[base + 16] = (ushort_t)p1;
-          zF[base + 24] = (ushort_t)(p1 >> 16);
-        }
-      }
-    }
-    __syncthreads();
-    __builtin_amdgcn_s_setprio(1);
-#pragma unroll
-    for (int kt = 0; kt < 8; ++kt) {
-      bf16x8 af2[4], bw2[4];
-#pragma unroll
-      for (int mi = 0; mi < 4; ++mi)
-        af2[mi] = *(const bf16x8*)&zF[((mi * 32 + kt * 4 + g) * 16 + li) * 8];
-#pragma unroll
-      for (int ni = 0; ni < 4; ++ni)
-        bw2[ni] = *(const bf16x8*)(Wf2 +
-            (size_t)(((4 * w + ni) * 128 + 32 * q + kt * 4 + g) * 16 + li) * 8);
-#pragma unroll
-      for (int mi = 0; mi < 4; ++mi)
-#pragma unroll
-        for (int ni = 0; ni < 4; ++ni)
-          acc2[mi][ni] = __builtin_amdgcn_mfma_f32_16x16x32_bf16(
-              af2[mi], bw2[ni], acc2[mi][ni], 0, 0, 0);
-    }
-    __builtin_amdgcn_s_setprio(0);
-  }
-
-#pragma unroll
-  for (int mi = 0; mi < 4; ++mi) {
-#pragma unroll
-    for (int rg = 0; rg < 4; ++rg) {
-      const int row_l = 16 * mi + r_in + rg;
-      float s1 = 0.f, s2 = 0.f;
-#pragma unroll
-      for (int ni = 0; ni < 4; ++ni) {
-        const int cg = 64 * w + 16 * ni + c_in;
-        const float zv = acc2[mi][ni][rg] + bf2[cg] + y1r[mi][ni][rg];
-        acc2[mi][ni][rg] = zv;
-        s1 += zv;
-        s2 += zv * zv;
-      }
-#pragma unroll
-      for (int off = 1; off <= 8; off <<= 1) {
-        s1 += __shfl_xor(s1, off, 64);
-        s2 += __shfl_xor(s2, off, 64);
-      }
-      if (c_in == 0) {
-        red[w][0][row_l] = s1;
-        red[w][1][row_l] = s2;
-      }
-    }
-  }
-  __syncthreads();
-  float colsum[4] = {0.f, 0.f, 0.f, 0.f};
-#pragma unroll
-  for (int mi = 0; mi < 4; ++mi) {
-#pragma unroll
-    for (int rg = 0; rg < 4; ++rg) {
-      const int row_l = 16 * mi + r_in + rg;
-      const float S1 = red[0][0][row_l] + red[1][0][row_l] + red[2][0][row_l] + red[3][0][row_l];
-      const float S2 = red[0][1][row_l] + red[1][1][row_l] + red[2][1][row_l] + red[3][1][row_l];
-      const float m = S1 * (1.f / 256.f);
-      const float var = S2 * (1.f / 256.f) - m * m;
-      const float rs = rsqrtf(var + 1e-5f);
-#pragma unroll
-      for (int ni = 0; ni < 4; ++ni) {
-        const int cg = 64 * w + 16 * ni + c_in;
-        const float v = (acc2[mi][ni][rg] - m) * rs * ln2g[cg] + ln2b[cg];
-        if constexpr (LAST) {
-          colsum[ni] += v;
-        } else {
-          y32[(row0 + row_l) * 256 + cg] = v;
-        }
-      }
-    }
-  }
-  if constexpr (LAST) {
-#pragma unroll
-    for (int ni = 0; ni < 4; ++ni) {
-      float s = colsum[ni];
-      s += __shfl_xor(s, 16, 64);
-      s += __shfl_xor(s, 32, 64);
-      if (g == 0) pool[(size_t)b * 256 + 64 * w + 16 * ni + c_in] = s * (1.f / 64.f);
+        }
+      }
+      __syncthreads();
     }
   }
 }
@@ -826,27 +886,18 @@
     linkgemm_k<<<dim3(Bc / 128, 1, L_), 512, 0, stream>>>(
         hbuf, W2T16, link_b2, pe, y32, Bc);
 
-    for (int l = 0; l < NL_ - 1; ++l) {
-      layer_k<0><<<dim3(Bc, 1, 1), 256, 0, stream>>>(
-          y32,
-          Wqkv16 + (size_t)l * 768 * 256, bqkv + l * 768,
-          Wo16 + (size_t)l * 256 * 256, bo + l * 256,
-          ln1_g + l * 256, ln1_b + l * 256,
-          Wff116 + (size_t)l * 1024 * 256, bff1 + l * 1024,
-          Wff216 + (size_t)l * 256 * 1024, bff2 + l * 256,
-          ln2_g + l * 256, ln2_b + l * 256, nullptr);
-    }
-    {
-      const int l = NL_ - 1;
-      layer_k<1><<<dim3(Bc, 1, 1), 256, 0, stream>>>(
-          y32,
-          Wqkv16 + (size_t)l * 768 * 256, bqkv + l * 768,
-          Wo16 + (size_t)l * 256 * 256, bo + l * 256,
-          ln1_g + l * 256, ln1_b + l * 256,
-          Wff116 + (size_t)l * 1024 * 256, bff1 + l * 1024,
-          Wff216 + (size_t)l * 256 * 1024, bff2 + l * 256,
-          ln2_g + l * 256, ln2_b + l * 256, pooled + bs * T_);
-    }
+    layers2_k<0><<<dim3(Bc, 1, 1), 256, 0, stream>>>(
+        y32,
+        Wqkv16, bqkv, Wo16, bo, ln1_g, ln1_b,
+        Wff116, bff1, Wff216, bff2, ln2_g, ln2_b, nullptr);
+    layers2_k<1><<<dim3(Bc, 1, 1), 256, 0, stream>>>(
+        y32,
+        Wqkv16 + (size_t)2 * 768 * 256, bqkv + 2 * 768,
+        Wo16 + (size_t)2 * 256 * 256, bo + 2 * 256,
+        ln1_g + 2 * 256, ln1_b + 2 * 256,
+        Wff116 + (size_t)2 * 1024 * 256, bff1 + 2 * 1024,
+        Wff216 + (size_t)2 * 256 * 1024, bff2 + 2 * 256,
+        ln2_g + 2 * 256, ln2_b + 2 * 256, pooled + bs * T_);
   }
 
   headgemm_k<<<B_ / 64, 256, 0, stream>>>(pooled, head_W1, head_b1, hh);
```
